# Performance work log

Hardware: AMD Instinct MI355X
Metric: run time of the kernel (lower is better)

## Reference

```python
import jax, jax.numpy as jnp
import numpy as np

EPS = 1e-5


def setup_inputs() -> dict:
    key = jax.random.key(0)
    k1, k2, k3 = jax.random.split(key, 3)
    B, C, H, W = 64, 512, 28, 28
    G = 8
    x = jax.random.normal(k1, (B, C, H, W), dtype=jnp.float32)
    weight = jax.random.normal(k2, (G,), dtype=jnp.float32)
    bias = jax.random.normal(k3, (G,), dtype=jnp.float32)
    return {"x": x, "weight": weight, "bias": bias, "groups": G}


def reference(x, weight, bias, groups):
    B, C, H, W = x.shape
    G = groups
    cpg = C // G
    hw = H * W
    xg = x.reshape(B, G, cpg, hw)                       # [B,G,cpg,HW]
    # per-channel spatial mean
    means = jnp.mean(xg, axis=-1, keepdims=True)        # [B,G,cpg,1]
    # similarity map: dot product of each spatial vector with channel-mean vector
    s = jnp.sum(xg * means, axis=2)                     # [B,G,HW]
    # normalize s over spatial dim (population variance, eps=1e-5)
    mu = jnp.mean(s, axis=-1, keepdims=True)
    var = jnp.mean(jnp.square(s - mu), axis=-1, keepdims=True)
    t = (s - mu) * jax.lax.rsqrt(var + EPS)             # [B,G,HW]
    gate = jax.nn.sigmoid(t * weight[None, :, None] + bias[None, :, None])
    out = xg * gate[:, :, None, :]                      # broadcast gate over channels
    return out.reshape(B, C, H, W)
```

## Files before the change

kernel.cpp:

```cpp
#include <hip/hip_runtime.h>


#define HW    784
#define HW4   196
#define CPG   64
#define NG    8
#define K4    12
#define TAIL4 4

__global__ __launch_bounds__(1024, 4)
void sge_kernel(const float* __restrict__ x,
                const float* __restrict__ weight,
                const float* __restrict__ bias,
                float* __restrict__ out) {
    __shared__ float sbuf[16 * HW];
    __shared__ float redbuf[32];

    const int t    = threadIdx.x;
    const int c    = t >> 4;
    const int j    = t & 15;
    const int wave = t >> 6;
    const int lane = t & 63;

    const int bg = blockIdx.x;
    const int g  = bg & (NG - 1);
    const size_t base4 = (size_t)bg * (CPG * HW4) + (size_t)c * HW4;

    const float4* xp = (const float4*)x + base4;
    float4 v[K4 + 1];
#pragma unroll
    for (int k = 0; k < K4; ++k) v[k] = xp[j + 16 * k];
    v[K4] = (j < TAIL4) ? xp[192 + j] : make_float4(0.f, 0.f, 0.f, 0.f);
#pragma unroll
    for (int k = 0; k <= K4; ++k)
        asm volatile("" : "+v"(v[k].x), "+v"(v[k].y), "+v"(v[k].z), "+v"(v[k].w));

    float cs = 0.f;
#pragma unroll
    for (int k = 0; k <= K4; ++k) cs += (v[k].x + v[k].y) + (v[k].z + v[k].w);
    cs += __shfl_xor(cs, 1, 64);
    cs += __shfl_xor(cs, 2, 64);
    cs += __shfl_xor(cs, 4, 64);
    cs += __shfl_xor(cs, 8, 64);
    const float mean_c = cs * (1.0f / (float)HW);

    float4* srow = (float4*)(sbuf + wave * HW);
#pragma unroll
    for (int k = 0; k <= K4; ++k) {
        float4 w;
        w.x = v[k].x * mean_c; w.y = v[k].y * mean_c;
        w.z = v[k].z * mean_c; w.w = v[k].w * mean_c;
        w.x += __shfl_xor(w.x, 16, 64); w.x += __shfl_xor(w.x, 32, 64);
        w.y += __shfl_xor(w.y, 16, 64); w.y += __shfl_xor(w.y, 32, 64);
        w.z += __shfl_xor(w.z, 16, 64); w.z += __shfl_xor(w.z, 32, 64);
        w.w += __shfl_xor(w.w, 16, 64); w.w += __shfl_xor(w.w, 32, 64);
        if (k < K4) {
            if (lane < 16) srow[j + 16 * k] = w;
        } else {
            if (lane < TAIL4) srow[192 + j] = w;
        }
    }
    __syncthreads();

    float s = 0.f;
    if (t < HW) {
#pragma unroll
        for (int w = 0; w < 16; ++w) s += sbuf[w * HW + t];
    }

    float rs = s, rs2 = s * s;
#pragma unroll
    for (int m = 1; m < 64; m <<= 1) {
        rs  += __shfl_xor(rs,  m, 64);
        rs2 += __shfl_xor(rs2, m, 64);
    }
    if (lane == 0) { redbuf[wave] = rs; redbuf[16 + wave] = rs2; }
    __syncthreads();

    float sum_s = 0.f, sum_s2 = 0.f;
#pragma unroll
    for (int w = 0; w < 16; ++w) { sum_s += redbuf[w]; sum_s2 += redbuf[16 + w]; }
    const float mu   = sum_s * (1.0f / (float)HW);
    const float var  = sum_s2 * (1.0f / (float)HW) - mu * mu;
    const float rstd = rsqrtf(var + 1e-5f);

    const float wg  = weight[g];
    const float bgv = bias[g];
    if (t < HW) {
        const float z = (s - mu) * rstd * wg + bgv;
        sbuf[t] = 1.0f / (1.0f + __expf(-z));
    }
    __syncthreads();

    const float4* gate4 = (const float4*)sbuf;
    float4* op = (float4*)out + base4;
#pragma unroll
    for (int k = 0; k < K4; ++k) {
        const float4 gv = gate4[j + 16 * k];
        float4 o;
        o.x = v[k].x * gv.x; o.y = v[k].y * gv.y;
        o.z = v[k].z * gv.z; o.w = v[k].w * gv.w;
        op[j + 16 * k] = o;
    }
    if (j < TAIL4) {
        const float4 gv = gate4[192 + j];
        float4 o;
        o.x = v[K4].x * gv.x; o.y = v[K4].y * gv.y;
        o.z = v[K4].z * gv.z; o.w = v[K4].w * gv.w;
        op[192 + j] = o;
    }
}

extern "C" void kernel_launch(void* const* d_in, const int* in_sizes, int n_in,
                              void* d_out, int out_size, void* d_ws, size_t ws_size,
                              hipStream_t stream) {
    const float* x      = (const float*)d_in[0];
    const float* weight = (const float*)d_in[1];
    const float* bias   = (const float*)d_in[2];
    float* out = (float*)d_out;
    sge_kernel<<<dim3(512), dim3(1024), 0, stream>>>(x, weight, bias, out);
}
```

Baseline: 192.1 us.

## Split fused SGE kernel into partial-similarity and apply kernels over workspace

Replaces the single fused kernel, which held each group's data in registers, with two kernels. The first uses 1024 blocks, each covering half a group's channels, and writes partial similarity sums to workspace. The second combines the partials, normalizes, computes the gate, and re-reads x to apply it. This is meant to raise parallelism and cut per-block register and LDS pressure, at the cost of reading x twice, an extra kernel launch, and a workspace round trip.

```diff
diff --git a/kernel.cpp b/kernel.cpp
--- a/kernel.cpp
+++ b/kernel.cpp
@@ -3,18 +3,12 @@
 
 #define HW    784
 #define HW4   196
-#define CPG   64
+#define K4    12
 #define NG    8
-#define K4    12
-#define TAIL4 4
 
-__global__ __launch_bounds__(1024, 4)
-void sge_kernel(const float* __restrict__ x,
-                const float* __restrict__ weight,
-                const float* __restrict__ bias,
-                float* __restrict__ out) {
-    __shared__ float sbuf[16 * HW];
-    __shared__ float redbuf[32];
+__global__ __launch_bounds__(512, 4)
+void sge_partial_s(const float* __restrict__ x, float* __restrict__ ws) {
+    __shared__ float sbuf[8 * HW];
 
     const int t    = threadIdx.x;
     const int c    = t >> 4;
@@ -22,18 +16,16 @@
     const int wave = t >> 6;
     const int lane = t & 63;
 
-    const int bg = blockIdx.x;
-    const int g  = bg & (NG - 1);
-    const size_t base4 = (size_t)bg * (CPG * HW4) + (size_t)c * HW4;
+    const int bg   = blockIdx.x >> 1;
+    const int half = blockIdx.x & 1;
+    const size_t base4 = (size_t)bg * (64 * HW4) + (size_t)half * (32 * HW4)
+                       + (size_t)c * HW4;
 
     const float4* xp = (const float4*)x + base4;
     float4 v[K4 + 1];
 #pragma unroll
     for (int k = 0; k < K4; ++k) v[k] = xp[j + 16 * k];
-    v[K4] = (j < TAIL4) ? xp[192 + j] : make_float4(0.f, 0.f, 0.f, 0.f);
-#pragma unroll
-    for (int k = 0; k <= K4; ++k)
-        asm volatile("" : "+v"(v[k].x), "+v"(v[k].y), "+v"(v[k].z), "+v"(v[k].w));
+    v[K4] = (j < 4) ? xp[192 + j] : make_float4(0.f, 0.f, 0.f, 0.f);
 
     float cs = 0.f;
 #pragma unroll
@@ -57,16 +49,42 @@
         if (k < K4) {
             if (lane < 16) srow[j + 16 * k] = w;
         } else {
-            if (lane < TAIL4) srow[192 + j] = w;
+            if (lane < 4) srow[192 + j] = w;
         }
     }
     __syncthreads();
 
+    float* wrow = ws + (size_t)blockIdx.x * HW;
+    {
+        float s = 0.f;
+#pragma unroll
+        for (int w = 0; w < 8; ++w) s += sbuf[w * HW + t];
+        wrow[t] = s;
+    }
+    if (t < HW - 512) {
+        const int p = t + 512;
+        float s = 0.f;
+#pragma unroll
+        for (int w = 0; w < 8; ++w) s += sbuf[w * HW + p];
+        wrow[p] = s;
+    }
+}
+
+__global__ __launch_bounds__(1024, 4)
+void sge_apply(const float* __restrict__ x, const float* __restrict__ ws,
+               const float* __restrict__ weight, const float* __restrict__ bias,
+               float* __restrict__ out) {
+    __shared__ float gate[HW];
+    __shared__ float redbuf[32];
+
+    const int t    = threadIdx.x;
+    const int wave = t >> 6;
+    const int lane = t & 63;
+    const int bg   = blockIdx.x;
+    const int g    = bg & (NG - 1);
+
     float s = 0.f;
-    if (t < HW) {
-#pragma unroll
-        for (int w = 0; w < 16; ++w) s += sbuf[w * HW + t];
-    }
+    if (t < HW) s = ws[(size_t)(2 * bg) * HW + t] + ws[(size_t)(2 * bg + 1) * HW + t];
 
     float rs = s, rs2 = s * s;
 #pragma unroll
@@ -84,29 +102,33 @@
     const float var  = sum_s2 * (1.0f / (float)HW) - mu * mu;
     const float rstd = rsqrtf(var + 1e-5f);
 
-    const float wg  = weight[g];
-    const float bgv = bias[g];
     if (t < HW) {
-        const float z = (s - mu) * rstd * wg + bgv;
-        sbuf[t] = 1.0f / (1.0f + __expf(-z));
+        const float z = (s - mu) * rstd * weight[g] + bias[g];
+        gate[t] = 1.0f / (1.0f + __expf(-z));
     }
     __syncthreads();
 
-    const float4* gate4 = (const float4*)sbuf;
+    const int c = t >> 4;
+    const int j = t & 15;
+    const size_t base4 = (size_t)bg * (64 * HW4) + (size_t)c * HW4;
+    const float4* xp = (const float4*)x + base4;
     float4* op = (float4*)out + base4;
+    const float4* gate4 = (const float4*)gate;
 #pragma unroll
     for (int k = 0; k < K4; ++k) {
+        const float4 xv = xp[j + 16 * k];
         const float4 gv = gate4[j + 16 * k];
         float4 o;
-        o.x = v[k].x * gv.x; o.y = v[k].y * gv.y;
-        o.z = v[k].z * gv.z; o.w = v[k].w * gv.w;
+        o.x = xv.x * gv.x; o.y = xv.y * gv.y;
+        o.z = xv.z * gv.z; o.w = xv.w * gv.w;
         op[j + 16 * k] = o;
     }
-    if (j < TAIL4) {
+    if (j < 4) {
+        const float4 xv = xp[192 + j];
         const float4 gv = gate4[192 + j];
         float4 o;
-        o.x = v[K4].x * gv.x; o.y = v[K4].y * gv.y;
-        o.z = v[K4].z * gv.z; o.w = v[K4].w * gv.w;
+        o.x = xv.x * gv.x; o.y = xv.y * gv.y;
+        o.z = xv.z * gv.z; o.w = xv.w * gv.w;
         op[192 + j] = o;
     }
 }
@@ -118,5 +140,8 @@
     const float* weight = (const float*)d_in[1];
     const float* bias   = (const float*)d_in[2];
     float* out = (float*)d_out;
-    sge_kernel<<<dim3(512), dim3(1024), 0, stream>>>(x, weight, bias, out);
+    float* ws  = (float*)d_ws;
+
+    sge_partial_s<<<dim3(1024), dim3(512), 0, stream>>>(x, ws);
+    sge_apply<<<dim3(512), dim3(1024), 0, stream>>>(x, ws, weight, bias, out);
 }
```

After: 211.3 us. +10.0%, slower.

## Split fused SGE kernel into partial-sum, gate, and apply kernels

Applied to the files above, without the earlier changes.

Replaces the single 1024-thread block-per-(batch,group) kernel with three kernels. The first computes partial similarity sums over 16-channel slices into workspace, the second reduces them and computes the sigmoid gate, and the third re-reads x and multiplies it by the gate using nontemporal loads and stores. This aims for more blocks and higher occupancy than the 512 large blocks with heavy shared-memory use. The cost is reading x twice from memory plus extra launches and workspace traffic.

```diff
diff --git a/kernel.cpp b/kernel.cpp
--- a/kernel.cpp
+++ b/kernel.cpp
@@ -3,18 +3,14 @@
 
 #define HW    784
 #define HW4   196
-#define CPG   64
+#define K4    12
 #define NG    8
-#define K4    12
-#define TAIL4 4
 
-__global__ __launch_bounds__(1024, 4)
-void sge_kernel(const float* __restrict__ x,
-                const float* __restrict__ weight,
-                const float* __restrict__ bias,
-                float* __restrict__ out) {
-    __shared__ float sbuf[16 * HW];
-    __shared__ float redbuf[32];
+typedef float v4f __attribute__((ext_vector_type(4)));
+
+__global__ __launch_bounds__(256, 4)
+void sge_partial_s(const float* __restrict__ x, float* __restrict__ ws) {
+    __shared__ float sbuf[4 * HW];
 
     const int t    = threadIdx.x;
     const int c    = t >> 4;
@@ -22,18 +18,16 @@
     const int wave = t >> 6;
     const int lane = t & 63;
 
-    const int bg = blockIdx.x;
-    const int g  = bg & (NG - 1);
-    const size_t base4 = (size_t)bg * (CPG * HW4) + (size_t)c * HW4;
+    const int bx   = blockIdx.x;
+    const int tile = bx >> 2;
+    const int q    = bx & 3;
+    const size_t base4 = (size_t)tile * (64 * HW4) + (size_t)(q * 16 + c) * HW4;
 
     const float4* xp = (const float4*)x + base4;
     float4 v[K4 + 1];
 #pragma unroll
     for (int k = 0; k < K4; ++k) v[k] = xp[j + 16 * k];
-    v[K4] = (j < TAIL4) ? xp[192 + j] : make_float4(0.f, 0.f, 0.f, 0.f);
-#pragma unroll
-    for (int k = 0; k <= K4; ++k)
-        asm volatile("" : "+v"(v[k].x), "+v"(v[k].y), "+v"(v[k].z), "+v"(v[k].w));
+    v[K4] = (j < 4) ? xp[192 + j] : make_float4(0.f, 0.f, 0.f, 0.f);
 
     float cs = 0.f;
 #pragma unroll
@@ -57,58 +51,88 @@
         if (k < K4) {
             if (lane < 16) srow[j + 16 * k] = w;
         } else {
-            if (lane < TAIL4) srow[192 + j] = w;
+            if (lane < 4) srow[192 + j] = w;
         }
     }
     __syncthreads();
 
-    float s = 0.f;
-    if (t < HW) {
+    float* wrow = ws + (size_t)bx * HW;
 #pragma unroll
-        for (int w = 0; w < 16; ++w) s += sbuf[w * HW + t];
+    for (int m = 0; m < 3; ++m) {
+        const int p = t + 256 * m;
+        float s = sbuf[p] + sbuf[HW + p] + sbuf[2 * HW + p] + sbuf[3 * HW + p];
+        wrow[p] = s;
     }
+    if (t < HW - 768) {
+        const int p = t + 768;
+        float s = sbuf[p] + sbuf[HW + p] + sbuf[2 * HW + p] + sbuf[3 * HW + p];
+        wrow[p] = s;
+    }
+}
 
-    float rs = s, rs2 = s * s;
+__global__ __launch_bounds__(256, 4)
+void sge_gate(const float* __restrict__ ws, const float* __restrict__ weight,
+              const float* __restrict__ bias, float* __restrict__ gbuf) {
+    __shared__ float redbuf[8];
+
+    const int t    = threadIdx.x;
+    const int wave = t >> 6;
+    const int lane = t & 63;
+    const int tile = blockIdx.x;
+    const int g    = tile & (NG - 1);
+    const float* wsA = ws + (size_t)(tile * 4) * HW;
+
+    float sv[4];
+    float rs = 0.f, rs2 = 0.f;
+#pragma unroll
+    for (int m = 0; m < 4; ++m) {
+        const int p = t + 256 * m;
+        float s = 0.f;
+        if (m < 3 || t < HW - 768)
+            s = wsA[p] + wsA[HW + p] + wsA[2 * HW + p] + wsA[3 * HW + p];
+        sv[m] = s;
+        rs += s; rs2 += s * s;
+    }
 #pragma unroll
     for (int m = 1; m < 64; m <<= 1) {
         rs  += __shfl_xor(rs,  m, 64);
         rs2 += __shfl_xor(rs2, m, 64);
     }
-    if (lane == 0) { redbuf[wave] = rs; redbuf[16 + wave] = rs2; }
+    if (lane == 0) { redbuf[wave] = rs; redbuf[4 + wave] = rs2; }
     __syncthreads();
 
-    float sum_s = 0.f, sum_s2 = 0.f;
-#pragma unroll
-    for (int w = 0; w < 16; ++w) { sum_s += redbuf[w]; sum_s2 += redbuf[16 + w]; }
+    float sum_s = redbuf[0] + redbuf[1] + redbuf[2] + redbuf[3];
+    float sum_s2 = redbuf[4] + redbuf[5] + redbuf[6] + redbuf[7];
     const float mu   = sum_s * (1.0f / (float)HW);
     const float var  = sum_s2 * (1.0f / (float)HW) - mu * mu;
     const float rstd = rsqrtf(var + 1e-5f);
+    const float wg   = weight[g];
+    const float bgv  = bias[g];
 
-    const float wg  = weight[g];
-    const float bgv = bias[g];
-    if (t < HW) {
-        const float z = (s - mu) * rstd * wg + bgv;
-        sbuf[t] = 1.0f / (1.0f + __expf(-z));
+    float* grow = gbuf + (size_t)tile * HW;
+#pragma unroll
+    for (int m = 0; m < 4; ++m) {
+        const int p = t + 256 * m;
+        if (m < 3 || t < HW - 768) {
+            const float z = (sv[m] - mu) * rstd * wg + bgv;
+            grow[p] = 1.0f / (1.0f + __expf(-z));
+        }
     }
-    __syncthreads();
+}
 
-    const float4* gate4 = (const float4*)sbuf;
-    float4* op = (float4*)out + base4;
-#pragma unroll
-    for (int k = 0; k < K4; ++k) {
-        const float4 gv = gate4[j + 16 * k];
-        float4 o;
-        o.x = v[k].x * gv.x; o.y = v[k].y * gv.y;
-        o.z = v[k].z * gv.z; o.w = v[k].w * gv.w;
-        op[j + 16 * k] = o;
-    }
-    if (j < TAIL4) {
-        const float4 gv = gate4[192 + j];
-        float4 o;
-        o.x = v[K4].x * gv.x; o.y = v[K4].y * gv.y;
-        o.z = v[K4].z * gv.z; o.w = v[K4].w * gv.w;
-        op[192 + j] = o;
-    }
+__global__ __launch_bounds__(256, 8)
+void sge_apply(const float* __restrict__ x, const float* __restrict__ gbuf,
+               float* __restrict__ out) {
+    const int  t    = threadIdx.x;
+    const int  tile = blockIdx.y;
+    const int  i4   = blockIdx.x * 256 + t;
+    const int  p4   = i4 % HW4;
+
+    const size_t idx = (size_t)tile * (64 * HW4) + i4;
+    const v4f xv = __builtin_nontemporal_load(&((const v4f*)x)[idx]);
+    const v4f gv = ((const v4f*)(gbuf + (size_t)tile * HW))[p4];
+    const v4f o  = xv * gv;
+    __builtin_nontemporal_store(o, &((v4f*)out)[idx]);
 }
 
 extern "C" void kernel_launch(void* const* d_in, const int* in_sizes, int n_in,
@@ -117,6 +141,11 @@
     const float* x      = (const float*)d_in[0];
     const float* weight = (const float*)d_in[1];
     const float* bias   = (const float*)d_in[2];
-    float* out = (float*)d_out;
-    sge_kernel<<<dim3(512), dim3(1024), 0, stream>>>(x, weight, bias, out);
+    float* out  = (float*)d_out;
+    float* ws   = (float*)d_ws;
+    float* gbuf = ws + (size_t)2048 * HW;
+
+    sge_partial_s<<<dim3(2048), dim3(256), 0, stream>>>(x, ws);
+    sge_gate<<<dim3(512), dim3(256), 0, stream>>>(ws, weight, bias, gbuf);
+    sge_apply<<<dim3(49, 512), dim3(256), 0, stream>>>(x, gbuf, out);
 }
```

New measurement: 202.3 us. +5.3%, slower.
